# Kernel tuning notes

Hardware: AMD Instinct MI355X
Metric: run time of the kernel (lower is better)

Reference implementation:

```python
import jax, jax.numpy as jnp
import numpy as np

N, C_IN, C_OUT, H = 4096, 1024, 512, 4
D = C_OUT // H  # per-head output dim
TEMP = 1.0


def setup_inputs() -> dict:
    key = jax.random.key(0)
    ks = jax.random.split(key, 6)
    node_feats = jax.random.normal(ks[0], (N, C_IN), dtype=jnp.float32)
    # sparse 0/1 adjacency mask, avg degree ~ 0.02*N
    adj_matrix = jax.random.bernoulli(ks[1], 0.02, (N, N)).astype(jnp.float32)
    lim_w = np.sqrt(6.0 / (C_IN + D))
    lim_v = np.sqrt(6.0 / (D + 1))
    W = jax.random.uniform(ks[2], (H, C_IN, D), jnp.float32, -lim_w, lim_w)
    b = jnp.zeros((H, D), dtype=jnp.float32)
    v0 = jax.random.uniform(ks[3], (H, D), jnp.float32, -lim_v, lim_v)
    v1 = jax.random.uniform(ks[4], (H, D), jnp.float32, -lim_v, lim_v)
    return {"node_feats": node_feats, "adj_matrix": adj_matrix,
            "W": W, "b": b, "v0": v0, "v1": v1}


def reference(node_feats, adj_matrix, W, b, v0, v1):
    # per-head linear projection: [H, N, D]
    h = jnp.einsum('nc,hcd->hnd', node_feats, W) + b[:, None, :]
    f1 = jnp.einsum('hnd,hd->hn', h, v0)  # [H, N]
    f2 = jnp.einsum('hnd,hd->hn', h, v1)  # [H, N]
    logits = adj_matrix[None, :, :] * (f1[:, :, None] + f2[:, None, :])
    # torch to_sparse drops exact zeros; sparse.softmax normalizes over
    # the remaining (nonzero) entries only, zeros stay zero when densified.
    mask = logits != 0
    vals = (jax.nn.sigmoid(logits) - 0.5) / TEMP
    rowmax = jnp.max(jnp.where(mask, vals, -1e30), axis=-1, keepdims=True)
    e = jnp.where(mask, jnp.exp(vals - rowmax), 0.0)
    denom = jnp.sum(e, axis=-1, keepdims=True)
    p = jnp.where(denom > 0, e / jnp.maximum(denom, 1e-30), 0.0)
    out = jnp.einsum('hnm,hmd->hnd', p, h)  # [H, N, D]
    # concat heads along feature dim -> [N, H*D]
    return out.transpose(1, 0, 2).reshape(node_feats.shape[0], -1)
```

## Files before the change

### kernel.cpp

```cpp
#include <hip/hip_runtime.h>
#include <hip/hip_bf16.h>

#define N_NODES 4096
#define C_IN    1024
#define H_HEADS 4
#define D_HEAD  128
#define C_OUT   512
#define DEG_CAP 256

typedef __attribute__((ext_vector_type(8))) short short8;
typedef __attribute__((ext_vector_type(8))) unsigned short u16x8;
typedef __attribute__((ext_vector_type(4))) float f32x4;

__device__ __forceinline__ unsigned short f2bf(float f) {
    unsigned u = __float_as_uint(f);
    u += 0x7FFFu + ((u >> 16) & 1u);
    return (unsigned short)(u >> 16);
}
__device__ __forceinline__ float bf2f(unsigned short u) {
    return __uint_as_float((unsigned)u << 16);
}
__device__ __forceinline__ float sigv(float s) {
    return 1.f / (1.f + __expf(-s)) - 0.5f;
}

#define GLOAD_LDS16(gp, lp)                                                        \
    __builtin_amdgcn_global_load_lds(                                              \
        (const __attribute__((address_space(1))) unsigned int*)(gp),               \
        (__attribute__((address_space(3))) unsigned int*)(lp), 16, 0, 0)

__global__ void k_cvt(const float* __restrict__ X, const float* __restrict__ W,
                      unsigned short* __restrict__ Xb, unsigned short* __restrict__ Wt,
                      float* __restrict__ F12) {
    if (blockIdx.x < 2048) {
        int g = blockIdx.x * blockDim.x + threadIdx.x;
        const float4* s = (const float4*)(X + (size_t)g * 8);
        float4 a = s[0], b = s[1];
        ushort4 p0, p1;
        p0.x = f2bf(a.x); p0.y = f2bf(a.y); p0.z = f2bf(a.z); p0.w = f2bf(a.w);
        p1.x = f2bf(b.x); p1.y = f2bf(b.y); p1.z = f2bf(b.z); p1.w = f2bf(b.w);
        ushort4* d = (ushort4*)(Xb + (size_t)g * 8);
        d[0] = p0; d[1] = p1;
    } else if (blockIdx.x < 2560) {
        int g = (blockIdx.x - 2048) * blockDim.x + threadIdx.x;
        int o = g * 4;
        int c  = o & 1023;
        int hd = o >> 10;
        int d  = hd & 127;
        int h  = hd >> 7;
        const float* src = W + (size_t)h * C_IN * D_HEAD + (size_t)c * D_HEAD + d;
        ushort4 p;
        p.x = f2bf(src[0 * D_HEAD]);
        p.y = f2bf(src[1 * D_HEAD]);
        p.z = f2bf(src[2 * D_HEAD]);
        p.w = f2bf(src[3 * D_HEAD]);
        *(ushort4*)(Wt + o) = p;
    } else {
        int g = (blockIdx.x - 2560) * blockDim.x + threadIdx.x;
        *(f32x4*)(F12 + (size_t)g * 4) = (f32x4){0.f, 0.f, 0.f, 0.f};
    }
}

__global__ void k_work(const unsigned short* __restrict__ Xb,
                       const unsigned short* __restrict__ Wt,
                       const float* __restrict__ bias,
                       const float* __restrict__ v0, const float* __restrict__ v1,
                       const float* __restrict__ adj,
                       unsigned short* __restrict__ Hb,
                       float* __restrict__ F1, float* __restrict__ F2,
                       unsigned short* __restrict__ idx, int* __restrict__ nnz) {
    __shared__ __align__(16) unsigned char smem[32768];
    const int t    = threadIdx.x;
    const int lane = t & 63;
    const int wid  = t >> 6;

    if (blockIdx.x < 512) {
        unsigned short* ldsA = (unsigned short*)smem;
        unsigned short* ldsB = ldsA + 2 * 64 * 64;
        const int wrow = wid >> 1, wcol = wid & 1;
        const int bid  = blockIdx.x;
        const int lin  = (bid & 7) * 64 + (bid >> 3);
        const int rowStart = (lin >> 3) * 64;
        const int colStart = (lin & 7) * 64;

        f32x4 acc[2][2];
#pragma unroll
        for (int m = 0; m < 2; ++m)
#pragma unroll
            for (int n = 0; n < 2; ++n) acc[m][n] = (f32x4){0.f, 0.f, 0.f, 0.f};

        const int lrow = lane >> 2;
        const int lkq  = (lane & 3) ^ ((lane >> 3) & 3);

        auto stage = [&](int buf, int k0) {
#pragma unroll
            for (int ii = 0; ii < 2; ++ii) {
                int c  = wid * 2 + ii;
                int h  = c >> 2, rb = c & 3;
                const unsigned short* g =
                    Xb + (size_t)(rowStart + rb * 16 + lrow) * C_IN + k0 + h * 32 + lkq * 8;
                GLOAD_LDS16(g, ldsA + buf * 4096 + h * 2048 + rb * 512);
            }
#pragma unroll
            for (int ii = 0; ii < 2; ++ii) {
                int c  = wid * 2 + ii;
                int h  = c >> 2, db = c & 3;
                const unsigned short* g =
                    Wt + (size_t)(colStart + db * 16 + lrow) * C_IN + k0 + h * 32 + lkq * 8;
                GLOAD_LDS16(g, ldsB + buf * 4096 + h * 2048 + db * 512);
            }
        };

        stage(0, 0);
        __syncthreads();

        const int fr = lane & 15;
        const int sw = ((lane >> 4) ^ ((fr >> 1) & 3)) * 8;
        int cur = 0;
        for (int kt = 0; kt < 16; ++kt) {
            if (kt < 15) stage(cur ^ 1, (kt + 1) * 64);
            const unsigned short* __restrict__ lA = ldsA + cur * 4096;
            const unsigned short* __restrict__ lB = ldsB + cur * 4096;
#pragma unroll
            for (int h = 0; h < 2; ++h) {
                short8 bfr[2];
#pragma unroll
                for (int n = 0; n < 2; ++n)
                    bfr[n] = *(const short8*)(lB + h * 2048 + (wcol * 32 + n * 16 + fr) * 32 + sw);
#pragma unroll
                for (int m = 0; m < 2; ++m) {
                    short8 a = *(const short8*)(lA + h * 2048 + (wrow * 32 + m * 16 + fr) * 32 + sw);
#pragma unroll
                    for (int n = 0; n < 2; ++n)
                        acc[m][n] = __builtin_amdgcn_mfma_f32_16x16x32_bf16(a, bfr[n], acc[m][n], 0, 0, 0);
                }
            }
            __syncthreads();
            cur ^= 1;
        }

        const int c0 = colStart + wcol * 32 + (lane & 15);
        const int c1 = c0 + 16;
        const int head = c0 >> 7;
        const float bb0 = bias[c0], bb1 = bias[c1];
        const float v0c0 = v0[c0], v0c1 = v0[c1];
        const float v1c0 = v1[c0], v1c1 = v1[c1];
#pragma unroll
        for (int m = 0; m < 2; ++m) {
            int row_g = rowStart + wrow * 32 + m * 16 + (lane >> 4) * 4;
#pragma unroll
            for (int r = 0; r < 4; ++r) {
                float h0 = acc[m][0][r] + bb0;
                float h1 = acc[m][1][r] + bb1;
                Hb[(size_t)(row_g + r) * C_OUT + c0] = f2bf(h0);
                Hb[(size_t)(row_g + r) * C_OUT + c1] = f2bf(h1);
                float p1 = h0 * v0c0 + h1 * v0c1;
                float p2 = h0 * v1c0 + h1 * v1c1;
#pragma unroll
                for (int off = 8; off; off >>= 1) {
                    p1 += __shfl_xor(p1, off);
                    p2 += __shfl_xor(p2, off);
                }
                if ((lane & 15) == 0) {
                    atomicAdd(&F1[(row_g + r) * 4 + head], p1);
                    atomicAdd(&F2[(row_g + r) * 4 + head], p2);
                }
            }
        }
    } else {
        int* wtot = (int*)smem;
        const int i = blockIdx.x - 512;
        const float4* arow = (const float4*)(adj + (size_t)i * N_NODES);
        float4 av[4];
#pragma unroll
        for (int r = 0; r < 4; ++r) av[r] = arow[r * 256 + t];

        int cnt = 0;
#pragma unroll
        for (int r = 0; r < 4; ++r)
            cnt += (av[r].x != 0.f) + (av[r].y != 0.f) + (av[r].z != 0.f) + (av[r].w != 0.f);
        int v = cnt;
#pragma unroll
        for (int off = 1; off < 64; off <<= 1) {
            int u = __shfl_up(v, off);
            if (lane >= off) v += u;
        }
        if (lane == 63) wtot[wid] = v;
        __syncthreads();
        int wpre = 0, total = 0;
#pragma unroll
        for (int w = 0; w < 4; ++w) {
            int tw = wtot[w];
            if (w < wid) wpre += tw;
            total += tw;
        }
        int off = wpre + v - cnt;
        unsigned short* ir = idx + (size_t)i * DEG_CAP;
#pragma unroll
        for (int r = 0; r < 4; ++r) {
            int j0 = (r * 256 + t) * 4;
            if (av[r].x != 0.f) { if (off < DEG_CAP) ir[off] = (unsigned short)j0;       off++; }
            if (av[r].y != 0.f) { if (off < DEG_CAP) ir[off] = (unsigned short)(j0 + 1); off++; }
            if (av[r].z != 0.f) { if (off < DEG_CAP) ir[off] = (unsigned short)(j0 + 2); off++; }
            if (av[r].w != 0.f) { if (off < DEG_CAP) ir[off] = (unsigned short)(j0 + 3); off++; }
        }
        if (t == 0) nnz[i] = min(total, DEG_CAP);
    }
}

__global__ void k_pv(const unsigned short* __restrict__ idx, const int* __restrict__ nnz,
                     const float* __restrict__ F1, const float* __restrict__ F2,
                     const unsigned short* __restrict__ Hb, float* __restrict__ Out) {
    __shared__ unsigned short jl[DEG_CAP];
    __shared__ float ev[DEG_CAP * 4];
    __shared__ float partial[4][C_OUT];
    __shared__ float dred[4][4];

    const int i    = blockIdx.x;
    const int t    = threadIdx.x;
    const int lane = t & 63;
    const int wid  = t >> 6;
    const int headl = lane >> 4;

    const int nv = nnz[i];
    float4 f1v = *(const float4*)(F1 + i * 4);
    const unsigned short* __restrict__ ji = idx + (size_t)i * DEG_CAP;

    float e0 = 0.f, e1 = 0.f, e2 = 0.f, e3 = 0.f;
    if (t < nv) {
        int j = ji[t];
        jl[t] = (unsigned short)j;
        float4 f2v = *(const float4*)(F2 + j * 4);
        float s0 = f1v.x + f2v.x, s1 = f1v.y + f2v.y;
        float s2 = f1v.z + f2v.z, s3 = f1v.w + f2v.w;
        e0 = (s0 != 0.f) ? __expf(sigv(s0)) : 0.f;
        e1 = (s1 != 0.f) ? __expf(sigv(s1)) : 0.f;
        e2 = (s2 != 0.f) ? __expf(sigv(s2)) : 0.f;
        e3 = (s3 != 0.f) ? __expf(sigv(s3)) : 0.f;
        ev[t * 4 + 0] = e0; ev[t * 4 + 1] = e1;
        ev[t * 4 + 2] = e2; ev[t * 4 + 3] = e3;
    }
#pragma unroll
    for (int o2 = 32; o2; o2 >>= 1) {
        e0 += __shfl_xor(e0, o2); e1 += __shfl_xor(e1, o2);
        e2 += __shfl_xor(e2, o2); e3 += __shfl_xor(e3, o2);
    }
    if (lane == 0) {
        dred[wid][0] = e0; dred[wid][1] = e1; dred[wid][2] = e2; dred[wid][3] = e3;
    }
    __syncthreads();

    float acc0[8], acc1[8];
#pragma unroll
    for (int k = 0; k < 8; ++k) { acc0[k] = 0.f; acc1[k] = 0.f; }
    const unsigned short* __restrict__ hp = Hb + lane * 8;

    int jj = wid;
#pragma unroll 4
    for (; jj + 4 < nv; jj += 8) {
        int ja = jl[jj], jb = jl[jj + 4];
        float ea = ev[jj * 4 + headl];
        float eb = ev[(jj + 4) * 4 + headl];
        u16x8 ha = *(const u16x8*)(hp + (size_t)ja * C_OUT);
        u16x8 hb = *(const u16x8*)(hp + (size_t)jb * C_OUT);
#pragma unroll
        for (int k = 0; k < 8; ++k) acc0[k] += ea * bf2f(ha[k]);
#pragma unroll
        for (int k = 0; k < 8; ++k) acc1[k] += eb * bf2f(hb[k]);
    }
    if (jj < nv) {
        int ja = jl[jj];
        float ea = ev[jj * 4 + headl];
        u16x8 ha = *(const u16x8*)(hp + (size_t)ja * C_OUT);
#pragma unroll
        for (int k = 0; k < 8; ++k) acc0[k] += ea * bf2f(ha[k]);
    }

    f32x4 lo = {acc0[0] + acc1[0], acc0[1] + acc1[1], acc0[2] + acc1[2], acc0[3] + acc1[3]};
    f32x4 hi = {acc0[4] + acc1[4], acc0[5] + acc1[5], acc0[6] + acc1[6], acc0[7] + acc1[7]};
    *(f32x4*)&partial[wid][lane * 8]     = lo;
    *(f32x4*)&partial[wid][lane * 8 + 4] = hi;
    __syncthreads();

    int head = t >> 6;
    float dn = dred[0][head] + dred[1][head] + dred[2][head] + dred[3][head];
    int c = 2 * t;
    float s0 = partial[0][c] + partial[1][c] + partial[2][c] + partial[3][c];
    float s1 = partial[0][c + 1] + partial[1][c + 1] + partial[2][c + 1] + partial[3][c + 1];
    float2 o;
    if (dn > 0.f) {
        float inv = 1.f / fmaxf(dn, 1e-30f);
        o.x = s0 * inv;
        o.y = s1 * inv;
    } else {
        o.x = 0.f; o.y = 0.f;
    }
    *(float2*)(Out + (size_t)i * C_OUT + c) = o;
}

extern "C" void kernel_launch(void* const* d_in, const int* in_sizes, int n_in,
                              void* d_out, int out_size, void* d_ws, size_t ws_size,
                              hipStream_t stream) {
    const float* X   = (const float*)d_in[0];
    const float* adj = (const float*)d_in[1];
    const float* W   = (const float*)d_in[2];
    const float* b   = (const float*)d_in[3];
    const float* v0  = (const float*)d_in[4];
    const float* v1  = (const float*)d_in[5];
    float* out = (float*)d_out;

    char* ws = (char*)d_ws;
    unsigned short* Wt  = (unsigned short*)ws;
    unsigned short* Xb  = (unsigned short*)(ws + (size_t)1 * 1024 * 1024);
    unsigned short* Hb  = (unsigned short*)(ws + (size_t)9 * 1024 * 1024);
    float*          F1  = (float*)(ws + (size_t)13 * 1024 * 1024);
    float*          F2  = F1 + N_NODES * 4;
    unsigned short* idx = (unsigned short*)(ws + (size_t)14 * 1024 * 1024);
    int*            nnz = (int*)(ws + (size_t)16 * 1024 * 1024);

    k_cvt<<<2592, 256, 0, stream>>>(X, W, Xb, Wt, F1);
    k_work<<<512 + N_NODES, 256, 0, stream>>>(Xb, Wt, b, v0, v1, adj, Hb, F1, F2, idx, nnz);
    k_pv<<<N_NODES, 256, 0, stream>>>(idx, nnz, F1, F2, Hb, out);
}
```

Before: 58.57 us.

## Assign one head per wave in k_pv to drop cross-wave LDS reduction

```diff
diff --git a/kernel.cpp b/kernel.cpp
--- a/kernel.cpp
+++ b/kernel.cpp
@@ -212,90 +212,66 @@
                      const float* __restrict__ F1, const float* __restrict__ F2,
                      const unsigned short* __restrict__ Hb, float* __restrict__ Out) {
     __shared__ unsigned short jl[DEG_CAP];
-    __shared__ float ev[DEG_CAP * 4];
-    __shared__ float partial[4][C_OUT];
-    __shared__ float dred[4][4];
+    __shared__ float ev[H_HEADS][DEG_CAP];
 
     const int i    = blockIdx.x;
     const int t    = threadIdx.x;
     const int lane = t & 63;
-    const int wid  = t >> 6;
-    const int headl = lane >> 4;
+    const int w    = t >> 6;
 
     const int nv = nnz[i];
-    float4 f1v = *(const float4*)(F1 + i * 4);
-    const unsigned short* __restrict__ ji = idx + (size_t)i * DEG_CAP;
-
-    float e0 = 0.f, e1 = 0.f, e2 = 0.f, e3 = 0.f;
-    if (t < nv) {
-        int j = ji[t];
-        jl[t] = (unsigned short)j;
-        float4 f2v = *(const float4*)(F2 + j * 4);
-        float s0 = f1v.x + f2v.x, s1 = f1v.y + f2v.y;
-        float s2 = f1v.z + f2v.z, s3 = f1v.w + f2v.w;
-        e0 = (s0 != 0.f) ? __expf(sigv(s0)) : 0.f;
-        e1 = (s1 != 0.f) ? __expf(sigv(s1)) : 0.f;
-        e2 = (s2 != 0.f) ? __expf(sigv(s2)) : 0.f;
-        e3 = (s3 != 0.f) ? __expf(sigv(s3)) : 0.f;
-        ev[t * 4 + 0] = e0; ev[t * 4 + 1] = e1;
-        ev[t * 4 + 2] = e2; ev[t * 4 + 3] = e3;
-    }
-#pragma unroll
-    for (int o2 = 32; o2; o2 >>= 1) {
-        e0 += __shfl_xor(e0, o2); e1 += __shfl_xor(e1, o2);
-        e2 += __shfl_xor(e2, o2); e3 += __shfl_xor(e3, o2);
-    }
-    if (lane == 0) {
-        dred[wid][0] = e0; dred[wid][1] = e1; dred[wid][2] = e2; dred[wid][3] = e3;
-    }
-    __syncthreads();
-
-    float acc0[8], acc1[8];
-#pragma unroll
-    for (int k = 0; k < 8; ++k) { acc0[k] = 0.f; acc1[k] = 0.f; }
-    const unsigned short* __restrict__ hp = Hb + lane * 8;
-
-    int jj = wid;
+
+    ushort4 jv = *(const ushort4*)(idx + (size_t)i * DEG_CAP + 4 * lane);
+    *(ushort4*)(jl + 4 * lane) = jv;
+
+    const float f1h = F1[i * 4 + w];
+    float dsum = 0.f;
+#pragma unroll
+    for (int s = 0; s < 4; ++s) {
+        int e = lane + 64 * s;
+        float ee = 0.f;
+        if (e < nv) {
+            int j = jl[e];
+            float sg = f1h + F2[j * 4 + w];
+            ee = (sg != 0.f) ? __expf(sigv(sg)) : 0.f;
+        }
+        ev[w][e] = ee;
+        dsum += ee;
+    }
+#pragma unroll
+    for (int o2 = 32; o2; o2 >>= 1) dsum += __shfl_xor(dsum, o2);
+
+    const unsigned short* __restrict__ hp = Hb + (size_t)w * D_HEAD + 2 * lane;
+    float a0 = 0.f, a1 = 0.f, b0 = 0.f, b1 = 0.f;
+    int jj = 0;
 #pragma unroll 4
-    for (; jj + 4 < nv; jj += 8) {
-        int ja = jl[jj], jb = jl[jj + 4];
-        float ea = ev[jj * 4 + headl];
-        float eb = ev[(jj + 4) * 4 + headl];
-        u16x8 ha = *(const u16x8*)(hp + (size_t)ja * C_OUT);
-        u16x8 hb = *(const u16x8*)(hp + (size_t)jb * C_OUT);
-#pragma unroll
-        for (int k = 0; k < 8; ++k) acc0[k] += ea * bf2f(ha[k]);
-#pragma unroll
-        for (int k = 0; k < 8; ++k) acc1[k] += eb * bf2f(hb[k]);
+    for (; jj + 1 < nv; jj += 2) {
+        int ja = jl[jj], jb = jl[jj + 1];
+        float ea = ev[w][jj], eb = ev[w][jj + 1];
+        unsigned pa = *(const unsigned*)(hp + (size_t)ja * C_OUT);
+        unsigned pb = *(const unsigned*)(hp + (size_t)jb * C_OUT);
+        a0 += ea * bf2f((unsigned short)(pa & 0xFFFFu));
+        a1 += ea * bf2f((unsigned short)(pa >> 16));
+        b0 += eb * bf2f((unsigned short)(pb & 0xFFFFu));
+        b1 += eb * bf2f((unsigned short)(pb >> 16));
     }
     if (jj < nv) {
         int ja = jl[jj];
-        float ea = ev[jj * 4 + headl];
-        u16x8 ha = *(const u16x8*)(hp + (size_t)ja * C_OUT);
-#pragma unroll
-        for (int k = 0; k < 8; ++k) acc0[k] += ea * bf2f(ha[k]);
-    }
-
-    f32x4 lo = {acc0[0] + acc1[0], acc0[1] + acc1[1], acc0[2] + acc1[2], acc0[3] + acc1[3]};
-    f32x4 hi = {acc0[4] + acc1[4], acc0[5] + acc1[5], acc0[6] + acc1[6], acc0[7] + acc1[7]};
-    *(f32x4*)&partial[wid][lane * 8]     = lo;
-    *(f32x4*)&partial[wid][lane * 8 + 4] = hi;
-    __syncthreads();
-
-    int head = t >> 6;
-    float dn = dred[0][head] + dred[1][head] + dred[2][head] + dred[3][head];
-    int c = 2 * t;
-    float s0 = partial[0][c] + partial[1][c] + partial[2][c] + partial[3][c];
-    float s1 = partial[0][c + 1] + partial[1][c + 1] + partial[2][c + 1] + partial[3][c + 1];
+        float ea = ev[w][jj];
+        unsigned pa = *(const unsigned*)(hp + (size_t)ja * C_OUT);
+        a0 += ea * bf2f((unsigned short)(pa & 0xFFFFu));
+        a1 += ea * bf2f((unsigned short)(pa >> 16));
+    }
+
     float2 o;
-    if (dn > 0.f) {
-        float inv = 1.f / fmaxf(dn, 1e-30f);
-        o.x = s0 * inv;
-        o.y = s1 * inv;
+    if (dsum > 0.f) {
+        float inv = 1.f / fmaxf(dsum, 1e-30f);
+        o.x = (a0 + b0) * inv;
+        o.y = (a1 + b1) * inv;
     } else {
         o.x = 0.f; o.y = 0.f;
     }
-    *(float2*)(Out + (size_t)i * C_OUT + c) = o;
+    *(float2*)(Out + (size_t)i * C_OUT + w * D_HEAD + 2 * lane) = o;
 }
 
 extern "C" void kernel_launch(void* const* d_in, const int* in_sizes, int n_in,
```

Measured after the change: 59.70 us. No clear change (+1.9%).
